# Kernel tuning notes

Measured on AMD Instinct MI355X. Metric: run time of the kernel, lower is better.

The kernel has to match this reference:

```python
import jax, jax.numpy as jnp
import numpy as np

# Module constants (from init_kwargs)
D_MODEL = 2048
N_HEAD = 16
D_HEAD = D_MODEL // N_HEAD  # 128
CH = N_HEAD + D_HEAD        # 144
R_Q, R_K, R_V = 6, 2, 2
ROPE_BASE = 10000.0
B, T = 2, 2048


def _rotary(b, cache_len):
    # b: [B, T, R, dh]; rotary applied in factor space, positions offset by cache_len
    dh = b.shape[-1]
    inv_freq = (1.0 / ROPE_BASE) ** (jnp.arange(0, dh, 2, dtype=jnp.float32) / dh)
    t = jnp.arange(b.shape[1], dtype=jnp.float32) + cache_len
    freqs = t[:, None] * inv_freq[None, :]             # [T, dh/2]
    cos = jnp.cos(freqs)[None, :, None, :]
    sin = jnp.sin(freqs)[None, :, None, :]
    x1, x2 = jnp.split(b, 2, axis=-1)
    y1 = x1 * cos + x2 * sin
    y2 = -x1 * sin + x2 * cos
    return jnp.concatenate([y1, y2], axis=-1).astype(b.dtype)


def setup_inputs() -> dict:
    key = jax.random.key(0)
    k0, k1, k2, k3 = jax.random.split(key, 4)
    s = 1.0 / np.sqrt(D_MODEL)
    return {
        "x": jax.random.normal(k0, (B, T, D_MODEL), dtype=jnp.float32),
        "W_q": jax.random.normal(k1, (R_Q * CH, D_MODEL), dtype=jnp.float32) * s,
        "W_kv": jax.random.normal(k2, ((R_K + R_V) * CH, D_MODEL), dtype=jnp.float32) * s,
        "W_o": jax.random.normal(k3, (D_MODEL, D_MODEL), dtype=jnp.float32) * s,
    }


def reference(x, W_q, W_kv, W_o):
    Bx, Tx, D = x.shape
    nh, dh = N_HEAD, D_HEAD
    cache_len = 0  # empty cache, full prefill

    # Factorized Q projection: [B,T,r_Q,ch]
    abq = (x @ W_q.T).reshape(Bx, Tx, R_Q, CH)
    a_q, b_q = abq[..., :nh], abq[..., nh:]

    # Factorized KV projection, rotary in factor space on the b-part
    abkv = (x @ W_kv.T).reshape(Bx, Tx, R_K + R_V, CH)
    a_kv = abkv[..., :nh]
    b_kv = _rotary(abkv[..., nh:], cache_len)

    a_k, b_k = a_kv[:, :, :R_K], b_kv[:, :, :R_K]
    a_v, b_v = a_kv[:, :, R_K:], b_kv[:, :, R_K:]

    # Rank-r outer-product reconstruction: [B,T,nh,dh]
    q = jnp.einsum("btrh,btrd->bthd", a_q, b_q) * (1.0 / R_Q)
    k = jnp.einsum("btrh,btrd->bthd", a_k, b_k) * (1.0 / R_K)
    v = jnp.einsum("btrh,btrd->bthd", a_v, b_v) * (1.0 / R_V)

    # Causal attention (flex_attention default scale = 1/sqrt(dh))
    scale = 1.0 / np.sqrt(dh)
    scores = jnp.einsum("bqhd,bkhd->bhqk", q, k) * scale
    qi = jnp.arange(Tx)[:, None]
    ki = jnp.arange(Tx)[None, :]
    causal = ki <= qi + cache_len
    scores = jnp.where(causal[None, None], scores, jnp.finfo(scores.dtype).min)
    attn = jax.nn.softmax(scores, axis=-1)
    y = jnp.einsum("bhqk,bkhd->bqhd", attn, v).reshape(Bx, Tx, D)
    return y @ W_o.T
```

## Files before the change

### kernel.cpp

```cpp
#include <hip/hip_runtime.h>
#include <hip/hip_bf16.h>
#include <cstdint>
#include <cstddef>

#define T_SEQ   2048
#define BATCH   2
#define DMODEL  2048
#define NHEAD   16
#define DHEAD   128
#define CH      144
#define RQ      6
#define RKV     4
#define N1      1440
#define N1P     1536
#define MROWS   4096

typedef short bf16x8 __attribute__((ext_vector_type(8)));
typedef float f32x4  __attribute__((ext_vector_type(4)));

#if defined(__has_builtin)
#  if __has_builtin(__builtin_amdgcn_exp2f)
#    define EXP2(x) __builtin_amdgcn_exp2f(x)
#  else
#    define EXP2(x) exp2f(x)
#  endif
#else
#  define EXP2(x) exp2f(x)
#endif

__device__ __forceinline__ float bflo(unsigned u){ return __uint_as_float(u << 16); }
__device__ __forceinline__ float bfhi(unsigned u){ return __uint_as_float(u & 0xffff0000u); }
__device__ __forceinline__ unsigned short f2bf(float f){
  unsigned b = __float_as_uint(f);
  b += 0x7fffu + ((b >> 16) & 1u);
  return (unsigned short)(b >> 16);
}

__global__ void cast_f32_bf16(const float* __restrict__ src, unsigned short* __restrict__ dst, int n4){
  int i = blockIdx.x * blockDim.x + threadIdx.x;
  int stride = gridDim.x * blockDim.x;
  for (; i < n4; i += stride){
    float4 v = ((const float4*)src)[i];
    ushort4 o;
    o.x = f2bf(v.x); o.y = f2bf(v.y); o.z = f2bf(v.z); o.w = f2bf(v.w);
    ((ushort4*)dst)[i] = o;
  }
}

__global__ void zero_u16(unsigned short* __restrict__ dst, int n){
  int i = blockIdx.x * blockDim.x + threadIdx.x;
  if (i < n) dst[i] = 0;
}

#define GBK 32
__global__ __launch_bounds__(256) void gemm_bt(const unsigned short* __restrict__ A,
                                               const unsigned short* __restrict__ Bm,
                                               float* __restrict__ C,
                                               int M, int N, int K){
  __shared__ __align__(16) unsigned short As[128 * GBK];
  __shared__ __align__(16) unsigned short Bs[128 * GBK];
  const int tid  = threadIdx.x;
  const int lane = tid & 63;
  const int wv   = tid >> 6;
  const int m0   = blockIdx.y * 128;
  const int n0   = blockIdx.x * 128;
  const int wm   = wv >> 1, wn = wv & 1;

  f32x4 acc[4][4];
#pragma unroll
  for (int i = 0; i < 4; ++i)
#pragma unroll
    for (int j = 0; j < 4; ++j) acc[i][j] = (f32x4){0.f, 0.f, 0.f, 0.f};

  const int srow = lane >> 2;
  const int scol = (lane & 3) * 8;
  const int kq   = (lane >> 4) * 8;
  const int rA   = lane & 15;

  for (int kt = 0; kt < K; kt += GBK){
#pragma unroll
    for (int i = 0; i < 2; ++i){
      int j = wv * 2 + i;
      int r = j * 16 + srow;
      const unsigned short* ga = A  + (size_t)(m0 + r) * K + kt + scol;
      const unsigned short* gb = Bm + (size_t)(n0 + r) * K + kt + scol;
      __builtin_amdgcn_global_load_lds((const __attribute__((address_space(1))) void*)ga,
                                       (__attribute__((address_space(3))) void*)&As[j * 16 * GBK], 16, 0, 0);
      __builtin_amdgcn_global_load_lds((const __attribute__((address_space(1))) void*)gb,
                                       (__attribute__((address_space(3))) void*)&Bs[j * 16 * GBK], 16, 0, 0);
    }
    __syncthreads();

    bf16x8 af[4], bfv[4];
#pragma unroll
    for (int mi = 0; mi < 4; ++mi)
      af[mi] = *(const bf16x8*)&As[(wm * 64 + mi * 16 + rA) * GBK + kq];
#pragma unroll
    for (int ni = 0; ni < 4; ++ni)
      bfv[ni] = *(const bf16x8*)&Bs[(wn * 64 + ni * 16 + rA) * GBK + kq];
#pragma unroll
    for (int mi = 0; mi < 4; ++mi)
#pragma unroll
      for (int ni = 0; ni < 4; ++ni)
        acc[mi][ni] = __builtin_amdgcn_mfma_f32_16x16x32_bf16(af[mi], bfv[ni], acc[mi][ni], 0, 0, 0);
    __syncthreads();
  }

#pragma unroll
  for (int mi = 0; mi < 4; ++mi)
#pragma unroll
    for (int ni = 0; ni < 4; ++ni){
      int row = m0 + wm * 64 + mi * 16 + (lane >> 4) * 4;
      int col = n0 + wn * 64 + ni * 16 + (lane & 15);
#pragma unroll
      for (int r = 0; r < 4; ++r)
        C[(size_t)(row + r) * N + col] = acc[mi][ni][r];
    }
}

__global__ __launch_bounds__(256) void qkv_kernel(const float* __restrict__ ab,
                                                  unsigned short* __restrict__ qb,
                                                  unsigned short* __restrict__ kb,
                                                  unsigned short* __restrict__ vb){
  __shared__ float sab[N1];
  const int bt = blockIdx.x;
  const int b  = bt >> 11;
  const int t  = bt & 2047;
  const float* row = ab + (size_t)bt * N1P;
  for (int j = threadIdx.x; j < N1; j += 256) sab[j] = row[j];
  __syncthreads();

  {
    int r = threadIdx.x >> 6;
    int d = threadIdx.x & 63;
    float inv = exp2f(-(float)d * 0.20762050593046f);
    float fr  = (float)t * inv;
    float c = cosf(fr), s = sinf(fr);
    float x1 = sab[864 + r * CH + 16 + d];
    float x2 = sab[864 + r * CH + 16 + 64 + d];
    sab[864 + r * CH + 16 + d]      = x1 * c + x2 * s;
    sab[864 + r * CH + 16 + 64 + d] = x2 * c - x1 * s;
  }
  __syncthreads();

  const int h  = threadIdx.x >> 4;
  const int d0 = (threadIdx.x & 15) * 8;

  {
    float aq[RQ];
#pragma unroll
    for (int r = 0; r < RQ; ++r) aq[r] = sab[r * CH + h];
    union { unsigned short u16[8]; uint4 v; } pk;
#pragma unroll
    for (int j = 0; j < 8; ++j){
      float acc = 0.f;
#pragma unroll
      for (int r = 0; r < RQ; ++r) acc += aq[r] * sab[r * CH + 16 + d0 + j];
      pk.u16[j] = f2bf(acc * (1.f / 6.f));
    }
    *(uint4*)&qb[((size_t)(b * 16 + h) * T_SEQ + t) * DHEAD + d0] = pk.v;
  }
  {
    float a0 = sab[864 + 0 * CH + h], a1 = sab[864 + 1 * CH + h];
    union { unsigned short u16[8]; uint4 v; } pk;
#pragma unroll
    for (int j = 0; j < 8; ++j){
      float acc = a0 * sab[864 + 0 * CH + 16 + d0 + j] + a1 * sab[864 + 1 * CH + 16 + d0 + j];
      pk.u16[j] = f2bf(acc * 0.5f);
    }
    *(uint4*)&kb[((size_t)(b * 16 + h) * T_SEQ + t) * DHEAD + d0] = pk.v;
  }
  {
    float a0 = sab[864 + 2 * CH + h], a1 = sab[864 + 3 * CH + h];
    union { unsigned short u16[8]; uint4 v; } pk;
#pragma unroll
    for (int j = 0; j < 8; ++j){
      float acc = a0 * sab[864 + 2 * CH + 16 + d0 + j] + a1 * sab[864 + 3 * CH + 16 + d0 + j];
      pk.u16[j] = f2bf(acc * 0.5f);
    }
    *(uint4*)&vb[((size_t)(b * 16 + h) * T_SEQ + t) * DHEAD + d0] = pk.v;
  }
}

#define SCL 0.12752551286084110f
__global__ __launch_bounds__(256) void attn_mfma(const unsigned short* __restrict__ qg,
                                                 const unsigned short* __restrict__ kg,
                                                 const unsigned short* __restrict__ vg,
                                                 unsigned short* __restrict__ yg){
  __shared__ __align__(16) unsigned short Ks[2 * 64 * DHEAD];
  __shared__ __align__(16) unsigned short Vt[2 * DHEAD * 64];
  __shared__ __align__(16) unsigned short Ps[4 * 32 * 64];

  const int bi   = blockIdx.x;
  const int xcd  = bi & 7;
  const int slot = bi >> 3;
  const int bh   = (slot & 3) * 8 + xcd;
  const int pr   = slot >> 2;
  const int b    = bh >> 4;
  const int h    = bh & 15;
  const size_t base = (size_t)bh * T_SEQ * DHEAD;

  const int lane = threadIdx.x & 63;
  const int wv   = threadIdx.x >> 6;
  const int lo   = lane & 15;
  const int hi   = lane >> 4;

  for (int phase = 0; phase < 2; ++phase){
    const int qt    = phase ? pr : (15 - pr);
    const int q0    = qt * 128;
    const int qrow0 = q0 + wv * 32;

    bf16x8 qf[2][4];
#pragma unroll
    for (int qb2 = 0; qb2 < 2; ++qb2)
#pragma unroll
      for (int ds = 0; ds < 4; ++ds){
        uint4 u = *(const uint4*)(qg + base + (size_t)(qrow0 + qb2 * 16 + lo) * DHEAD + ds * 32 + hi * 8);
        unsigned w[4] = {u.x, u.y, u.z, u.w};
        union { unsigned short s[8]; bf16x8 v; } r;
#pragma unroll
        for (int q = 0; q < 4; ++q){
          r.s[2*q]   = f2bf(bflo(w[q]) * SCL);
          r.s[2*q+1] = f2bf(bfhi(w[q]) * SCL);
        }
        qf[qb2][ds] = r.v;
      }

    f32x4 o4[2][8];
#pragma unroll
    for (int qb2 = 0; qb2 < 2; ++qb2)
#pragma unroll
      for (int dcb = 0; dcb < 8; ++dcb) o4[qb2][dcb] = (f32x4){0.f,0.f,0.f,0.f};
    float mrow[2][4], lrow[2][4];
#pragma unroll
    for (int qb2 = 0; qb2 < 2; ++qb2)
#pragma unroll
      for (int r = 0; r < 4; ++r){ mrow[qb2][r] = -1e30f; lrow[qb2][r] = 0.f; }

    const int nt = 2 * qt + 2;

    {
#pragma unroll
      for (int i = 0; i < 4; ++i){
        int c    = (i * 4 + wv) * 64 + lane;
        int row  = c >> 4;
        int gcol = (c & 15) ^ (row & 7);
        const unsigned short* src = kg + base + (size_t)(0 * 64 + row) * DHEAD + gcol * 8;
        __builtin_amdgcn_global_load_lds((const __attribute__((address_space(1))) void*)src,
                                         (__attribute__((address_space(3))) void*)&Ks[(i * 4 + wv) * 512], 16, 0, 0);
      }
      uint4 tv[4];
#pragma unroll
      for (int i = 0; i < 4; ++i)
        tv[i] = *(const uint4*)(vg + base + (size_t)(0 * 64 + lane) * DHEAD + (i * 4 + wv) * 8);
#pragma unroll
      for (int i = 0; i < 4; ++i){
        int d0 = (i * 4 + wv) * 8;
        union { uint4 v; unsigned short u[8]; } t2; t2.v = tv[i];
#pragma unroll
        for (int j = 0; j < 8; ++j)
          Vt[(d0 + j) * 64 + (lane ^ (j << 3))] = t2.u[j];
      }
      __syncthreads();
    }

    for (int kt = 0; kt < nt; ++kt){
      const int cur = kt & 1;
      const int nxt = cur ^ 1;
      const bool pf = (kt + 1 < nt);
      uint4 tv[4];
      if (pf){
#pragma unroll
        for (int i = 0; i < 4; ++i){
          int c    = (i * 4 + wv) * 64 + lane;
          int row  = c >> 4;
          int gcol = (c & 15) ^ (row & 7);
          const unsigned short* src = kg + base + (size_t)((kt + 1) * 64 + row) * DHEAD + gcol * 8;
          __builtin_amdgcn_global_load_lds((const __attribute__((address_space(1))) void*)src,
                                           (__attribute__((address_space(3))) void*)&Ks[nxt * 8192 + (i * 4 + wv) * 512], 16, 0, 0);
        }
#pragma unroll
        for (int i = 0; i < 4; ++i)
          tv[i] = *(const uint4*)(vg + base + (size_t)((kt + 1) * 64 + lane) * DHEAD + (i * 4 + wv) * 8);
      }

      if (kt * 64 <= qrow0 + 31){
        const unsigned short* Kb = &Ks[cur * 8192];
        const unsigned short* Vb = &Vt[cur * 8192];

        f32x4 s4[2][4];
#pragma unroll
        for (int qb2 = 0; qb2 < 2; ++qb2)
#pragma unroll
          for (int cb = 0; cb < 4; ++cb) s4[qb2][cb] = (f32x4){0.f,0.f,0.f,0.f};
        __builtin_amdgcn_s_setprio(1);
#pragma unroll
        for (int ds = 0; ds < 4; ++ds){
          bf16x8 kf[4];
#pragma unroll
          for (int cb = 0; cb < 4; ++cb){
            int kvr = cb * 16 + lo;
            kf[cb] = *(const bf16x8*)&Kb[kvr * DHEAD + ((ds * 32 + hi * 8) ^ ((kvr & 7) << 3))];
          }
#pragma unroll
          for (int qb2 = 0; qb2 < 2; ++qb2)
#pragma unroll
            for (int cb = 0; cb < 4; ++cb)
              s4[qb2][cb] = __builtin_amdgcn_mfma_f32_16x16x32_bf16(qf[qb2][ds], kf[cb], s4[qb2][cb], 0, 0, 0);
        }
        __builtin_amdgcn_s_setprio(0);

        if (kt * 64 + 63 > qrow0){
#pragma unroll
          for (int qb2 = 0; qb2 < 2; ++qb2)
#pragma unroll
            for (int cb = 0; cb < 4; ++cb)
#pragma unroll
              for (int r = 0; r < 4; ++r){
                int kv = kt * 64 + cb * 16 + lo;
                int q  = qrow0 + qb2 * 16 + hi * 4 + r;
                if (kv > q) s4[qb2][cb][r] = -1e30f;
              }
        }

        float mx8[2][4];
#pragma unroll
        for (int qb2 = 0; qb2 < 2; ++qb2)
#pragma unroll
          for (int r = 0; r < 4; ++r){
            float mx = fmaxf(fmaxf(s4[qb2][0][r], s4[qb2][1][r]), fmaxf(s4[qb2][2][r], s4[qb2][3][r]));
            mx = fmaxf(mx, __shfl_xor(mx, 1));
            mx = fmaxf(mx, __shfl_xor(mx, 2));
            mx = fmaxf(mx, __shfl_xor(mx, 4));
            mx = fmaxf(mx, __shfl_xor(mx, 8));
            mx8[qb2][r] = mx;
          }
        bool grow = false;
#pragma unroll
        for (int qb2 = 0; qb2 < 2; ++qb2)
#pragma unroll
          for (int r = 0; r < 4; ++r) grow |= (mx8[qb2][r] > mrow[qb2][r] + 8.f);
        if (__any(grow)){
#pragma unroll
          for (int qb2 = 0; qb2 < 2; ++qb2)
#pragma unroll
            for (int r = 0; r < 4; ++r){
              float mN = fmaxf(mrow[qb2][r], mx8[qb2][r]);
              float alpha = EXP2(mrow[qb2][r] - mN);
              mrow[qb2][r] = mN;
              lrow[qb2][r] *= alpha;
#pragma unroll
              for (int dcb = 0; dcb < 8; ++dcb) o4[qb2][dcb][r] *= alpha;
            }
        }
#pragma unroll
        for (int qb2 = 0; qb2 < 2; ++qb2)
#pragma unroll
          for (int r = 0; r < 4; ++r){
            float m = mrow[qb2][r];
            float p0 = EXP2(s4[qb2][0][r] - m);
            float p1 = EXP2(s4[qb2][1][r] - m);
            float p2 = EXP2(s4[qb2][2][r] - m);
            float p3 = EXP2(s4[qb2][3][r] - m);
            float ps = p0 + p1 + p2 + p3;
            ps += __shfl_xor(ps, 1);
            ps += __shfl_xor(ps, 2);
            ps += __shfl_xor(ps, 4);
            ps += __shfl_xor(ps, 8);
            lrow[qb2][r] += ps;
            int qloc = qb2 * 16 + hi * 4 + r;
            int sw   = ((qloc + (qloc >> 3)) & 7) << 3;
            int pb   = wv * 2048 + qloc * 64;
            Ps[pb + ((0 * 16 + lo) ^ sw)] = f2bf(p0);
            Ps[pb + ((1 * 16 + lo) ^ sw)] = f2bf(p1);
            Ps[pb + ((2 * 16 + lo) ^ sw)] = f2bf(p2);
            Ps[pb + ((3 * 16 + lo) ^ sw)] = f2bf(p3);
          }

        asm volatile("s_waitcnt lgkmcnt(0)" ::: "memory");

        __builtin_amdgcn_s_setprio(1);
#pragma unroll
        for (int ks = 0; ks < 2; ++ks){
          bf16x8 pa[2];
#pragma unroll
          for (int qb2 = 0; qb2 < 2; ++qb2){
            int qloc = qb2 * 16 + lo;
            int sw   = ((qloc + (qloc >> 3)) & 7) << 3;
            pa[qb2] = *(const bf16x8*)&Ps[wv * 2048 + qloc * 64 + ((ks * 32 + hi * 8) ^ sw)];
          }
#pragma unroll
          for (int dcb = 0; dcb < 8; ++dcb){
            int d = dcb * 16 + lo;
            bf16x8 vf = *(const bf16x8*)&Vb[d * 64 + ((ks * 32 + hi * 8) ^ ((d & 7) << 3))];
#pragma unroll
            for (int qb2 = 0; qb2 < 2; ++qb2)
              o4[qb2][dcb] = __builtin_amdgcn_mfma_f32_16x16x32_bf16(pa[qb2], vf, o4[qb2][dcb], 0, 0, 0);
          }
        }
        __builtin_amdgcn_s_setprio(0);
      }

      if (pf){
#pragma unroll
        for (int i = 0; i < 4; ++i){
          int d0 = (i * 4 + wv) * 8;
          union { uint4 v; unsigned short u[8]; } t2; t2.v = tv[i];
#pragma unroll
          for (int j = 0; j < 8; ++j)
            Vt[nxt * 8192 + (d0 + j) * 64 + (lane ^ (j << 3))] = t2.u[j];
        }
      }
      __syncthreads();
    }

#pragma unroll
    for (int qb2 = 0; qb2 < 2; ++qb2)
#pragma unroll
      for (int r = 0; r < 4; ++r){
        float inv = 1.f / lrow[qb2][r];
        int q = qrow0 + qb2 * 16 + hi * 4 + r;
        size_t yb_ = ((size_t)(b * T_SEQ + q)) * DMODEL + h * DHEAD;
#pragma unroll
        for (int dcb = 0; dcb < 8; ++dcb)
          yg[yb_ + dcb * 16 + lo] = f2bf(o4[qb2][dcb][r] * inv);
      }
    __syncthreads();
  }
}

extern "C" void kernel_launch(void* const* d_in, const int* in_sizes, int n_in,
                              void* d_out, int out_size, void* d_ws, size_t ws_size,
                              hipStream_t stream) {
  const float* x   = (const float*)d_in[0];
  const float* Wq  = (const float*)d_in[1];
  const float* Wkv = (const float*)d_in[2];
  const float* Wo  = (const float*)d_in[3];
  float* out = (float*)d_out;

  char* ws = (char*)d_ws;
  size_t off = 0;
  auto alloc = [&](size_t bytes) -> void* {
    void* p = ws + off;
    off += (bytes + 255) & ~(size_t)255;
    return p;
  };
  unsigned short* xb = (unsigned short*)alloc((size_t)MROWS * DMODEL * 2);
  unsigned short* wc = (unsigned short*)alloc((size_t)N1P * DMODEL * 2);
  unsigned short* wo = (unsigned short*)alloc((size_t)DMODEL * DMODEL * 2);
  float*          abf = (float*)alloc((size_t)MROWS * N1P * 4);
  unsigned short* qb = (unsigned short*)alloc((size_t)MROWS * DMODEL * 2);
  unsigned short* kb = (unsigned short*)alloc((size_t)MROWS * DMODEL * 2);
  unsigned short* vb = (unsigned short*)alloc((size_t)MROWS * DMODEL * 2);
  unsigned short* yb = (unsigned short*)alloc((size_t)MROWS * DMODEL * 2);

  {
    int n4 = MROWS * DMODEL / 4;
    cast_f32_bf16<<<2048, 256, 0, stream>>>(x, xb, n4);
    n4 = RQ * CH * DMODEL / 4;
    cast_f32_bf16<<<1024, 256, 0, stream>>>(Wq, wc, n4);
    n4 = RKV * CH * DMODEL / 4;
    cast_f32_bf16<<<1024, 256, 0, stream>>>(Wkv, wc + (size_t)RQ * CH * DMODEL, n4);
    int npad = (N1P - N1) * DMODEL;
    zero_u16<<<(npad + 255) / 256, 256, 0, stream>>>(wc + (size_t)N1 * DMODEL, npad);
    n4 = DMODEL * DMODEL / 4;
    cast_f32_bf16<<<2048, 256, 0, stream>>>(Wo, wo, n4);
  }

  gemm_bt<<<dim3(N1P / 128, MROWS / 128), 256, 0, stream>>>(xb, wc, abf, MROWS, N1P, DMODEL);
  qkv_kernel<<<MROWS, 256, 0, stream>>>(abf, qb, kb, vb);
  attn_mfma<<<256, 256, 0, stream>>>(qb, kb, vb, yb);
  gemm_bt<<<dim3(DMODEL / 128, MROWS / 128), 256, 0, stream>>>(yb, wo, out, MROWS, DMODEL, DMODEL);
}
```

Before: 378.6 us.

## Split attention blocks into eight waves of sixteen query rows each

```diff
diff --git a/kernel.cpp b/kernel.cpp
--- a/kernel.cpp
+++ b/kernel.cpp
@@ -183,13 +183,13 @@
 }
 
 #define SCL 0.12752551286084110f
-__global__ __launch_bounds__(256) void attn_mfma(const unsigned short* __restrict__ qg,
+__global__ __launch_bounds__(512) void attn_mfma(const unsigned short* __restrict__ qg,
                                                  const unsigned short* __restrict__ kg,
                                                  const unsigned short* __restrict__ vg,
                                                  unsigned short* __restrict__ yg){
   __shared__ __align__(16) unsigned short Ks[2 * 64 * DHEAD];
   __shared__ __align__(16) unsigned short Vt[2 * DHEAD * 64];
-  __shared__ __align__(16) unsigned short Ps[4 * 32 * 64];
+  __shared__ __align__(16) unsigned short Ps[8 * 16 * 64];
 
   const int bi   = blockIdx.x;
   const int xcd  = bi & 7;
@@ -208,54 +208,48 @@
   for (int phase = 0; phase < 2; ++phase){
     const int qt    = phase ? pr : (15 - pr);
     const int q0    = qt * 128;
-    const int qrow0 = q0 + wv * 32;
-
-    bf16x8 qf[2][4];
-#pragma unroll
-    for (int qb2 = 0; qb2 < 2; ++qb2)
-#pragma unroll
-      for (int ds = 0; ds < 4; ++ds){
-        uint4 u = *(const uint4*)(qg + base + (size_t)(qrow0 + qb2 * 16 + lo) * DHEAD + ds * 32 + hi * 8);
-        unsigned w[4] = {u.x, u.y, u.z, u.w};
-        union { unsigned short s[8]; bf16x8 v; } r;
-#pragma unroll
-        for (int q = 0; q < 4; ++q){
-          r.s[2*q]   = f2bf(bflo(w[q]) * SCL);
-          r.s[2*q+1] = f2bf(bfhi(w[q]) * SCL);
-        }
-        qf[qb2][ds] = r.v;
-      }
-
-    f32x4 o4[2][8];
-#pragma unroll
-    for (int qb2 = 0; qb2 < 2; ++qb2)
-#pragma unroll
-      for (int dcb = 0; dcb < 8; ++dcb) o4[qb2][dcb] = (f32x4){0.f,0.f,0.f,0.f};
-    float mrow[2][4], lrow[2][4];
-#pragma unroll
-    for (int qb2 = 0; qb2 < 2; ++qb2)
-#pragma unroll
-      for (int r = 0; r < 4; ++r){ mrow[qb2][r] = -1e30f; lrow[qb2][r] = 0.f; }
+    const int qrow0 = q0 + wv * 16;
+
+    bf16x8 qf[4];
+#pragma unroll
+    for (int ds = 0; ds < 4; ++ds){
+      uint4 u = *(const uint4*)(qg + base + (size_t)(qrow0 + lo) * DHEAD + ds * 32 + hi * 8);
+      unsigned w[4] = {u.x, u.y, u.z, u.w};
+      union { unsigned short s[8]; bf16x8 v; } r;
+#pragma unroll
+      for (int q = 0; q < 4; ++q){
+        r.s[2*q]   = f2bf(bflo(w[q]) * SCL);
+        r.s[2*q+1] = f2bf(bfhi(w[q]) * SCL);
+      }
+      qf[ds] = r.v;
+    }
+
+    f32x4 o4[8];
+#pragma unroll
+    for (int dcb = 0; dcb < 8; ++dcb) o4[dcb] = (f32x4){0.f,0.f,0.f,0.f};
+    float mrow[4], lrow[4];
+#pragma unroll
+    for (int r = 0; r < 4; ++r){ mrow[r] = -1e30f; lrow[r] = 0.f; }
 
     const int nt = 2 * qt + 2;
 
     {
 #pragma unroll
-      for (int i = 0; i < 4; ++i){
-        int c    = (i * 4 + wv) * 64 + lane;
+      for (int i = 0; i < 2; ++i){
+        int c    = (i * 8 + wv) * 64 + lane;
         int row  = c >> 4;
         int gcol = (c & 15) ^ (row & 7);
-        const unsigned short* src = kg + base + (size_t)(0 * 64 + row) * DHEAD + gcol * 8;
+        const unsigned short* src = kg + base + (size_t)row * DHEAD + gcol * 8;
         __builtin_amdgcn_global_load_lds((const __attribute__((address_space(1))) void*)src,
-                                         (__attribute__((address_space(3))) void*)&Ks[(i * 4 + wv) * 512], 16, 0, 0);
-      }
-      uint4 tv[4];
-#pragma unroll
-      for (int i = 0; i < 4; ++i)
-        tv[i] = *(const uint4*)(vg + base + (size_t)(0 * 64 + lane) * DHEAD + (i * 4 + wv) * 8);
-#pragma unroll
-      for (int i = 0; i < 4; ++i){
-        int d0 = (i * 4 + wv) * 8;
+                                         (__attribute__((address_space(3))) void*)&Ks[(i * 8 + wv) * 512], 16, 0, 0);
+      }
+      uint4 tv[2];
+#pragma unroll
+      for (int i = 0; i < 2; ++i)
+        tv[i] = *(const uint4*)(vg + base + (size_t)lane * DHEAD + (i * 8 + wv) * 8);
+#pragma unroll
+      for (int i = 0; i < 2; ++i){
+        int d0 = (i * 8 + wv) * 8;
         union { uint4 v; unsigned short u[8]; } t2; t2.v = tv[i];
 #pragma unroll
         for (int j = 0; j < 8; ++j)
@@ -268,31 +262,29 @@
       const int cur = kt & 1;
       const int nxt = cur ^ 1;
       const bool pf = (kt + 1 < nt);
-      uint4 tv[4];
+      uint4 tv[2];
       if (pf){
 #pragma unroll
-        for (int i = 0; i < 4; ++i){
-          int c    = (i * 4 + wv) * 64 + lane;
+        for (int i = 0; i < 2; ++i){
+          int c    = (i * 8 + wv) * 64 + lane;
           int row  = c >> 4;
           int gcol = (c & 15) ^ (row & 7);
           const unsigned short* src = kg + base + (size_t)((kt + 1) * 64 + row) * DHEAD + gcol * 8;
           __builtin_amdgcn_global_load_lds((const __attribute__((address_space(1))) void*)src,
-                                           (__attribute__((address_space(3))) void*)&Ks[nxt * 8192 + (i * 4 + wv) * 512], 16, 0, 0);
-        }
-#pragma unroll
-        for (int i = 0; i < 4; ++i)
-          tv[i] = *(const uint4*)(vg + base + (size_t)((kt + 1) * 64 + lane) * DHEAD + (i * 4 + wv) * 8);
-      }
-
-      if (kt * 64 <= qrow0 + 31){
+                                           (__attribute__((address_space(3))) void*)&Ks[nxt * 8192 + (i * 8 + wv) * 512], 16, 0, 0);
+        }
+#pragma unroll
+        for (int i = 0; i < 2; ++i)
+          tv[i] = *(const uint4*)(vg + base + (size_t)((kt + 1) * 64 + lane) * DHEAD + (i * 8 + wv) * 8);
+      }
+
+      if (kt * 64 <= qrow0 + 15){
         const unsigned short* Kb = &Ks[cur * 8192];
         const unsigned short* Vb = &Vt[cur * 8192];
 
-        f32x4 s4[2][4];
-#pragma unroll
-        for (int qb2 = 0; qb2 < 2; ++qb2)
-#pragma unroll
-          for (int cb = 0; cb < 4; ++cb) s4[qb2][cb] = (f32x4){0.f,0.f,0.f,0.f};
+        f32x4 s4[4];
+#pragma unroll
+        for (int cb = 0; cb < 4; ++cb) s4[cb] = (f32x4){0.f,0.f,0.f,0.f};
         __builtin_amdgcn_s_setprio(1);
 #pragma unroll
         for (int ds = 0; ds < 4; ++ds){
@@ -303,99 +295,84 @@
             kf[cb] = *(const bf16x8*)&Kb[kvr * DHEAD + ((ds * 32 + hi * 8) ^ ((kvr & 7) << 3))];
           }
 #pragma unroll
-          for (int qb2 = 0; qb2 < 2; ++qb2)
-#pragma unroll
-            for (int cb = 0; cb < 4; ++cb)
-              s4[qb2][cb] = __builtin_amdgcn_mfma_f32_16x16x32_bf16(qf[qb2][ds], kf[cb], s4[qb2][cb], 0, 0, 0);
+          for (int cb = 0; cb < 4; ++cb)
+            s4[cb] = __builtin_amdgcn_mfma_f32_16x16x32_bf16(qf[ds], kf[cb], s4[cb], 0, 0, 0);
         }
         __builtin_amdgcn_s_setprio(0);
 
         if (kt * 64 + 63 > qrow0){
 #pragma unroll
-          for (int qb2 = 0; qb2 < 2; ++qb2)
-#pragma unroll
-            for (int cb = 0; cb < 4; ++cb)
-#pragma unroll
-              for (int r = 0; r < 4; ++r){
-                int kv = kt * 64 + cb * 16 + lo;
-                int q  = qrow0 + qb2 * 16 + hi * 4 + r;
-                if (kv > q) s4[qb2][cb][r] = -1e30f;
-              }
-        }
-
-        float mx8[2][4];
-#pragma unroll
-        for (int qb2 = 0; qb2 < 2; ++qb2)
+          for (int cb = 0; cb < 4; ++cb)
+#pragma unroll
+            for (int r = 0; r < 4; ++r){
+              int kv = kt * 64 + cb * 16 + lo;
+              int q  = qrow0 + hi * 4 + r;
+              if (kv > q) s4[cb][r] = -1e30f;
+            }
+        }
+
+        float mx8[4];
+#pragma unroll
+        for (int r = 0; r < 4; ++r){
+          float mx = fmaxf(fmaxf(s4[0][r], s4[1][r]), fmaxf(s4[2][r], s4[3][r]));
+          mx = fmaxf(mx, __shfl_xor(mx, 1));
+          mx = fmaxf(mx, __shfl_xor(mx, 2));
+          mx = fmaxf(mx, __shfl_xor(mx, 4));
+          mx = fmaxf(mx, __shfl_xor(mx, 8));
+          mx8[r] = mx;
+        }
+        bool grow = false;
+#pragma unroll
+        for (int r = 0; r < 4; ++r) grow |= (mx8[r] > mrow[r] + 8.f);
+        if (__any(grow)){
 #pragma unroll
           for (int r = 0; r < 4; ++r){
-            float mx = fmaxf(fmaxf(s4[qb2][0][r], s4[qb2][1][r]), fmaxf(s4[qb2][2][r], s4[qb2][3][r]));
-            mx = fmaxf(mx, __shfl_xor(mx, 1));
-            mx = fmaxf(mx, __shfl_xor(mx, 2));
-            mx = fmaxf(mx, __shfl_xor(mx, 4));
-            mx = fmaxf(mx, __shfl_xor(mx, 8));
-            mx8[qb2][r] = mx;
+            float mN = fmaxf(mrow[r], mx8[r]);
+            float alpha = EXP2(mrow[r] - mN);
+            mrow[r] = mN;
+            lrow[r] *= alpha;
+#pragma unroll
+            for (int dcb = 0; dcb < 8; ++dcb) o4[dcb][r] *= alpha;
           }
-        bool grow = false;
-#pragma unroll
-        for (int qb2 = 0; qb2 < 2; ++qb2)
-#pragma unroll
-          for (int r = 0; r < 4; ++r) grow |= (mx8[qb2][r] > mrow[qb2][r] + 8.f);
-        if (__any(grow)){
-#pragma unroll
-          for (int qb2 = 0; qb2 < 2; ++qb2)
-#pragma unroll
-            for (int r = 0; r < 4; ++r){
-              float mN = fmaxf(mrow[qb2][r], mx8[qb2][r]);
-              float alpha = EXP2(mrow[qb2][r] - mN);
-              mrow[qb2][r] = mN;
-              lrow[qb2][r] *= alpha;
-#pragma unroll
-              for (int dcb = 0; dcb < 8; ++dcb) o4[qb2][dcb][r] *= alpha;
-            }
-        }
-#pragma unroll
-        for (int qb2 = 0; qb2 < 2; ++qb2)
-#pragma unroll
-          for (int r = 0; r < 4; ++r){
-            float m = mrow[qb2][r];
-            float p0 = EXP2(s4[qb2][0][r] - m);
-            float p1 = EXP2(s4[qb2][1][r] - m);
-            float p2 = EXP2(s4[qb2][2][r] - m);
-            float p3 = EXP2(s4[qb2][3][r] - m);
-            float ps = p0 + p1 + p2 + p3;
-            ps += __shfl_xor(ps, 1);
-            ps += __shfl_xor(ps, 2);
-            ps += __shfl_xor(ps, 4);
-            ps += __shfl_xor(ps, 8);
-            lrow[qb2][r] += ps;
-            int qloc = qb2 * 16 + hi * 4 + r;
+        }
+#pragma unroll
+        for (int r = 0; r < 4; ++r){
+          float m = mrow[r];
+          float p0 = EXP2(s4[0][r] - m);
+          float p1 = EXP2(s4[1][r] - m);
+          float p2 = EXP2(s4[2][r] - m);
+          float p3 = EXP2(s4[3][r] - m);
+          float ps = p0 + p1 + p2 + p3;
+          ps += __shfl_xor(ps, 1);
+          ps += __shfl_xor(ps, 2);
+          ps += __shfl_xor(ps, 4);
+          ps += __shfl_xor(ps, 8);
+          lrow[r] += ps;
+          int qloc = hi * 4 + r;
+          int sw   = ((qloc + (qloc >> 3)) & 7) << 3;
+          int pb   = wv * 1024 + qloc * 64;
+          Ps[pb + ((0 * 16 + lo) ^ sw)] = f2bf(p0);
+          Ps[pb + ((1 * 16 + lo) ^ sw)] = f2bf(p1);
+          Ps[pb + ((2 * 16 + lo) ^ sw)] = f2bf(p2);
+          Ps[pb + ((3 * 16 + lo) ^ sw)] = f2bf(p3);
+        }
+
+        asm volatile("s_waitcnt lgkmcnt(0)" ::: "memory");
+
+        __builtin_amdgcn_s_setprio(1);
+#pragma unroll
+        for (int ks = 0; ks < 2; ++ks){
+          bf16x8 pa;
+          {
+            int qloc = lo;
             int sw   = ((qloc + (qloc >> 3)) & 7) << 3;
-            int pb   = wv * 2048 + qloc * 64;
-            Ps[pb + ((0 * 16 + lo) ^ sw)] = f2bf(p0);
-            Ps[pb + ((1 * 16 + lo) ^ sw)] = f2bf(p1);
-            Ps[pb + ((2 * 16 + lo) ^ sw)] = f2bf(p2);
-            Ps[pb + ((3 * 16 + lo) ^ sw)] = f2bf(p3);
-          }
-
-        asm volatile("s_waitcnt lgkmcnt(0)" ::: "memory");
-
-        __builtin_amdgcn_s_setprio(1);
-#pragma unroll
-        for (int ks = 0; ks < 2; ++ks){
-          bf16x8 pa[2];
-#pragma unroll
-          for (int qb2 = 0; qb2 < 2; ++qb2){
-            int qloc = qb2 * 16 + lo;
-            int sw   = ((qloc + (qloc >> 3)) & 7) << 3;
-            pa[qb2] = *(const bf16x8*)&Ps[wv * 2048 + qloc * 64 + ((ks * 32 + hi * 8) ^ sw)];
+            pa = *(const bf16x8*)&Ps[wv * 1024 + qloc * 64 + ((ks * 32 + hi * 8) ^ sw)];
           }
 #pragma unroll
           for (int dcb = 0; dcb < 8; ++dcb){
             int d = dcb * 16 + lo;
             bf16x8 vf = *(const bf16x8*)&Vb[d * 64 + ((ks * 32 + hi * 8) ^ ((d & 7) << 3))];
-#pragma unroll
-            for (int qb2 = 0; qb2 < 2; ++qb2)
-              o4[qb2][dcb] = __builtin_amdgcn_mfma_f32_16x16x32_bf16(pa[qb2], vf, o4[qb2][dcb], 0, 0, 0);
+            o4[dcb] = __builtin_amdgcn_mfma_f32_16x16x32_bf16(pa, vf, o4[dcb], 0, 0, 0);
           }
         }
         __builtin_amdgcn_s_setprio(0);
@@ -403,8 +380,8 @@
 
       if (pf){
 #pragma unroll
-        for (int i = 0; i < 4; ++i){
-          int d0 = (i * 4 + wv) * 8;
+        for (int i = 0; i < 2; ++i){
+          int d0 = (i * 8 + wv) * 8;
           union { uint4 v; unsigned short u[8]; } t2; t2.v = tv[i];
 #pragma unroll
           for (int j = 0; j < 8; ++j)
@@ -415,16 +392,14 @@
     }
 
 #pragma unroll
-    for (int qb2 = 0; qb2 < 2; ++qb2)
-#pragma unroll
-      for (int r = 0; r < 4; ++r){
-        float inv = 1.f / lrow[qb2][r];
-        int q = qrow0 + qb2 * 16 + hi * 4 + r;
-        size_t yb_ = ((size_t)(b * T_SEQ + q)) * DMODEL + h * DHEAD;
-#pragma unroll
-        for (int dcb = 0; dcb < 8; ++dcb)
-          yg[yb_ + dcb * 16 + lo] = f2bf(o4[qb2][dcb][r] * inv);
-      }
+    for (int r = 0; r < 4; ++r){
+      float inv = 1.f / lrow[r];
+      int q = qrow0 + hi * 4 + r;
+      size_t yb_ = ((size_t)(b * T_SEQ + q)) * DMODEL + h * DHEAD;
+#pragma unroll
+      for (int dcb = 0; dcb < 8; ++dcb)
+        yg[yb_ + dcb * 16 + lo] = f2bf(o4[dcb][r] * inv);
+    }
     __syncthreads();
   }
 }
@@ -469,6 +444,6 @@
 
   gemm_bt<<<dim3(N1P / 128, MROWS / 128), 256, 0, stream>>>(xb, wc, abf, MROWS, N1P, DMODEL);
   qkv_kernel<<<MROWS, 256, 0, stream>>>(abf, qb, kb, vb);
-  attn_mfma<<<256, 256, 0, stream>>>(qb, kb, vb, yb);
+  attn_mfma<<<256, 512, 0, stream>>>(qb, kb, vb, yb);
   gemm_bt<<<dim3(DMODEL / 128, MROWS / 128), 256, 0, stream>>>(yb, wo, out, MROWS, DMODEL, DMODEL);
 }
```

Measured after the change: 341.0 us. -9.9%, faster.
